# Optimization experiments

Measured on AMD Instinct MI355X. Metric: run time of the kernel, lower is better.

Reference implementation:

```python
import jax, jax.numpy as jnp
import numpy as np

B, T, E, H, R = 1, 2048, 4096, 16, 64
D = E // H
SCALE_ATTN = float(np.sqrt(D))


def _i8_linear(x, W, b, alpha, beta):
    # W8A8B8O8Linear: int8 in, int8 weight/bias, int8 out with requant epilogue
    acc = jnp.einsum('bte,oe->bto', x.astype(jnp.int32), W.astype(jnp.int32)).astype(jnp.float32)
    y = alpha * acc + beta * b.astype(jnp.float32)
    return jnp.clip(jnp.round(y), -128, 127).astype(jnp.int8)


def _rotate_every_two(x):
    x1, x2 = x[..., ::2], x[..., 1::2]
    return jnp.stack([-x2, x1], axis=-1).reshape(x.shape)


def _sincos(seq_len, dim):
    inv_freq = 1.0 / (10000.0 ** (jnp.arange(0, dim, 2, dtype=jnp.float32) / dim))
    ang = jnp.arange(seq_len, dtype=jnp.float32)[:, None] * inv_freq[None, :]
    return jnp.sin(ang), jnp.cos(ang)


def _apply_rotary(x, sin, cos):
    # duplicate_interleave -> repeat each freq twice along last dim
    sin = jnp.repeat(sin, 2, axis=-1)[None, :, None, :]
    cos = jnp.repeat(cos, 2, axis=-1)[None, :, None, :]
    return x * cos + _rotate_every_two(x) * sin


def setup_inputs():
    key = jax.random.key(0)
    ks = jax.random.split(key, 9)
    i8 = lambda k, s: jax.random.randint(k, s, -128, 128, dtype=jnp.int32).astype(jnp.int8)
    return {
        'hidden_states': i8(ks[0], (B, T, E)),
        'Wq': i8(ks[1], (E, E)), 'bq': i8(ks[2], (E,)),
        'Wk': i8(ks[3], (E, E)), 'bk': i8(ks[4], (E,)),
        'Wv': i8(ks[5], (E, E)), 'bv': i8(ks[6], (E,)),
        'Wo': i8(ks[7], (E, E)),
        'b_out': jax.random.normal(ks[8], (E,), dtype=jnp.float32),
        'alpha_q': 2e-4, 'beta_q': 1.0,
        'alpha_k': 2e-4, 'beta_k': 1.0,
        'alpha_v': 2e-4, 'beta_v': 1.0,
        'alpha_qk': 1e-3, 'alpha_pv': 1e-2, 'alpha_out': 2e-4,
    }


def reference(hidden_states, Wq, bq, Wk, bk, Wv, bv, Wo, b_out,
              alpha_q, beta_q, alpha_k, beta_k, alpha_v, beta_v,
              alpha_qk, alpha_pv, alpha_out):
    # int8 q/k/v projections -> [B, T, H, D]
    q = _i8_linear(hidden_states, Wq, bq, alpha_q, beta_q).reshape(B, T, H, D)
    k = _i8_linear(hidden_states, Wk, bk, alpha_k, beta_k).reshape(B, T, H, D)
    v = _i8_linear(hidden_states, Wv, bv, alpha_v, beta_v).reshape(B, T, H, D)
    v = v.transpose(0, 2, 1, 3)  # [B, H, T, D] int8

    # fused rotary on first R dims (float math on dequantized-per-tensor int8 codes)
    sin, cos = _sincos(T, R)
    qf, kf = q.astype(jnp.float32), k.astype(jnp.float32)
    qf = jnp.concatenate([_apply_rotary(qf[..., :R], sin, cos), qf[..., R:]], axis=-1)
    kf = jnp.concatenate([_apply_rotary(kf[..., :R], sin, cos), kf[..., R:]], axis=-1)
    # torch .to(int8) truncates toward zero
    to_i8 = lambda x: jnp.clip(jnp.trunc(x), -128, 127).astype(jnp.int8)
    q = to_i8(qf.transpose(0, 2, 1, 3))  # [B, H, T, D]
    k = to_i8(kf.transpose(0, 2, 1, 3))

    scores = alpha_qk * jnp.einsum('bhtd,bhsd->bhts', q.astype(jnp.int32), k.astype(jnp.int32)).astype(jnp.float32)
    causal = jnp.tril(jnp.ones((T, T), dtype=bool))
    scores = jnp.where(causal, scores, jnp.finfo(jnp.float32).min)
    probs = jax.nn.softmax(scores / SCALE_ATTN, axis=-1)
    probs = jnp.round(probs * 127.0).astype(jnp.int8)  # requant probs to int8

    acc = jnp.einsum('bhts,bhsd->bhtd', probs.astype(jnp.int32), v.astype(jnp.int32)).astype(jnp.float32)
    attn_out = jnp.clip(jnp.round(alpha_pv * acc), -128, 127).astype(jnp.int8)
    attn_out = attn_out.transpose(0, 2, 1, 3).reshape(B, T, E)  # merge heads

    # W8A8BFP32OFP32Linear
    out = alpha_out * jnp.einsum('bte,oe->bto', attn_out.astype(jnp.int32), Wo.astype(jnp.int32)).astype(jnp.float32) + b_out
    return out
```

## Files before the change

kernel.cpp:

```cpp
#include <hip/hip_runtime.h>
#include <cstdint>
#include <cmath>

#define T_ 2048
#define E_ 4096
#define H_ 16
#define D_ 256
#define NF 32

typedef int v4i  __attribute__((ext_vector_type(4)));

__device__ __forceinline__ int dot4(int a, int b, int c) {
#if __has_builtin(__builtin_amdgcn_sdot4)
  return __builtin_amdgcn_sdot4(a, b, c, false);
#else
  c += ((a << 24) >> 24) * ((b << 24) >> 24);
  c += ((a << 16) >> 24) * ((b << 16) >> 24);
  c += ((a <<  8) >> 24) * ((b <<  8) >> 24);
  c += (a >> 24) * (b >> 24);
  return c;
#endif
}

__device__ __forceinline__ int pack4i(int4 v) {
  return (v.x & 255) | ((v.y & 255) << 8) | ((v.z & 255) << 16) | (v.w << 24);
}

#define GLD_LDS16(g, l)                                                        \
  __builtin_amdgcn_global_load_lds(                                            \
      (const __attribute__((address_space(1))) void*)(g),                      \
      (__attribute__((address_space(3))) void*)(l), 16, 0, 0)

__global__ void sincos_kernel(float* __restrict__ sinT, float* __restrict__ cosT) {
  int idx = blockIdx.x * 256 + threadIdx.x;
  int t = idx >> 5, j = idx & 31;
  float invf = (float)exp(-(double)j * (log(10000.0) / 32.0));
  float ang = (float)t * invf;
  sinT[idx] = (float)sin((double)ang);
  cosT[idx] = (float)cos((double)ang);
}

__global__ __launch_bounds__(256) void repack_kernel(const int* __restrict__ src,
                                                     int8_t* __restrict__ dst) {
  size_t i = (size_t)blockIdx.x * 256 + threadIdx.x;
  const int4* s = (const int4*)src + i * 4;
  int4 a = s[0], b = s[1], c = s[2], d = s[3];
  int4 o;
  o.x = pack4i(a); o.y = pack4i(b); o.z = pack4i(c); o.w = pack4i(d);
  ((int4*)dst)[i] = o;
}

__global__ __launch_bounds__(256) void qkv_gemm_mfma(
    const int8_t* __restrict__ x8,
    const int8_t* __restrict__ Wq8, const int* __restrict__ bq,
    const int8_t* __restrict__ Wk8, const int* __restrict__ bk,
    const int8_t* __restrict__ Wv8, const int* __restrict__ bv,
    const float* __restrict__ alpq, const float* __restrict__ betq,
    const float* __restrict__ alpk, const float* __restrict__ betk,
    const float* __restrict__ alpv, const float* __restrict__ betv,
    int8_t* __restrict__ Q8, int8_t* __restrict__ K8, int8_t* __restrict__ VT)
{
  const int mode = blockIdx.z;
  const int8_t* __restrict__ W = (mode == 0) ? Wq8 : (mode == 1 ? Wk8 : Wv8);
  const int* __restrict__ bs   = (mode == 0) ? bq  : (mode == 1 ? bk  : bv);
  const float alpha = (mode == 0) ? alpq[0] : (mode == 1 ? alpk[0] : alpv[0]);
  const float beta  = (mode == 0) ? betq[0] : (mode == 1 ? betk[0] : betv[0]);

  __shared__ int8_t As[128 * 64];
  __shared__ int8_t Bs[128 * 64];

  const int tid  = threadIdx.x;
  const int wave = tid >> 6, lane = tid & 63;
  const int wm = wave >> 1, wn = wave & 1;
  const int t0 = blockIdx.x * 128, o0 = blockIdx.y * 128;

  const int srow = lane >> 2;
  const int scol = (lane & 3) * 16;
  const int col  = lane & 15;
  const int quad = lane >> 4;

  v4i acc[4][4] = {};

  const int8_t* gA0 = x8 + (size_t)(t0 + wave * 32 + srow) * E_ + scol;
  const int8_t* gB0 = W  + (size_t)(o0 + wave * 32 + srow) * E_ + scol;

  for (int e0 = 0; e0 < E_; e0 += 64) {
    __syncthreads();
    GLD_LDS16(gA0 + e0,                 As + wave * 2048);
    GLD_LDS16(gA0 + e0 + 16 * E_,       As + wave * 2048 + 1024);
    GLD_LDS16(gB0 + e0,                 Bs + wave * 2048);
    GLD_LDS16(gB0 + e0 + 16 * E_,       Bs + wave * 2048 + 1024);
    __syncthreads();

    v4i a[4], b[4];
    #pragma unroll
    for (int i = 0; i < 4; ++i)
      a[i] = *(const v4i*)(As + (wm * 64 + i * 16 + col) * 64 + quad * 16);
    #pragma unroll
    for (int j = 0; j < 4; ++j)
      b[j] = *(const v4i*)(Bs + (wn * 64 + j * 16 + col) * 64 + quad * 16);
    #pragma unroll
    for (int i = 0; i < 4; ++i)
      #pragma unroll
      for (int j = 0; j < 4; ++j)
        acc[i][j] = __builtin_amdgcn_mfma_i32_16x16x64_i8(a[i], b[j], acc[i][j], 0, 0, 0);
  }

  int8_t* __restrict__ dst = (mode == 0) ? Q8 : (mode == 1 ? K8 : VT);
  #pragma unroll
  for (int j = 0; j < 4; ++j) {
    const int o  = o0 + wn * 64 + j * 16 + col;
    const int h  = o >> 8;
    const int dd = o & 255;
    const float bb = (float)bs[o];
    #pragma unroll
    for (int i = 0; i < 4; ++i) {
      const int tb = t0 + wm * 64 + i * 16 + quad * 4;
      int qb[4];
      #pragma unroll
      for (int r = 0; r < 4; ++r) {
        float v = __fadd_rn(__fmul_rn(alpha, (float)acc[i][j][r]),
                            __fmul_rn(beta, bb));
        v = rintf(v);
        v = fminf(fmaxf(v, -128.0f), 127.0f);
        qb[r] = (int)v;
      }
      if (mode == 2) {
        int packed = (qb[0] & 255) | ((qb[1] & 255) << 8) |
                     ((qb[2] & 255) << 16) | ((qb[3] & 255) << 24);
        *(int*)(dst + ((size_t)h * 256 + dd) * T_ + tb) = packed;
      } else {
        #pragma unroll
        for (int r = 0; r < 4; ++r)
          dst[((size_t)h * T_ + tb + r) * D_ + dd] = (int8_t)qb[r];
      }
    }
  }
}

__global__ __launch_bounds__(256) void rope_kernel(
    int8_t* __restrict__ Q8, int8_t* __restrict__ K8,
    const float* __restrict__ sinT, const float* __restrict__ cosT)
{
  int idx = blockIdx.x * 256 + threadIdx.x;
  int c = idx & 3;
  int t = (idx >> 2) & (T_ - 1);
  int h = (idx >> 13) & (H_ - 1);
  int m = idx >> 17;
  int8_t* base = (m == 0 ? Q8 : K8) + ((size_t)h * T_ + t) * D_ + c * 16;
  int4 v = *(int4*)base;
  int u[4] = {v.x, v.y, v.z, v.w};
  const int jb = c * 8;
  #pragma unroll
  for (int ui = 0; ui < 4; ++ui) {
    const int j = jb + ui * 2;
    const float s0 = sinT[t * NF + j],     c0 = cosT[t * NF + j];
    const float s1 = sinT[t * NF + j + 1], c1 = cosT[t * NF + j + 1];
    const int w = u[ui];
    float y0 = (float)((w << 24) >> 24);
    float y1 = (float)((w << 16) >> 24);
    float y2 = (float)((w <<  8) >> 24);
    float y3 = (float)(w >> 24);
    float r0 = __fadd_rn(__fmul_rn(y0, c0), __fmul_rn(-y1, s0));
    float r1 = __fadd_rn(__fmul_rn(y1, c0), __fmul_rn( y0, s0));
    float r2 = __fadd_rn(__fmul_rn(y2, c1), __fmul_rn(-y3, s1));
    float r3 = __fadd_rn(__fmul_rn(y3, c1), __fmul_rn( y2, s1));
    int q0 = (int)fminf(fmaxf(truncf(r0), -128.0f), 127.0f);
    int q1 = (int)fminf(fmaxf(truncf(r1), -128.0f), 127.0f);
    int q2 = (int)fminf(fmaxf(truncf(r2), -128.0f), 127.0f);
    int q3 = (int)fminf(fmaxf(truncf(r3), -128.0f), 127.0f);
    u[ui] = (q0 & 255) | ((q1 & 255) << 8) | ((q2 & 255) << 16) | ((q3 & 255) << 24);
  }
  int4 ov; ov.x = u[0]; ov.y = u[1]; ov.z = u[2]; ov.w = u[3];
  *(int4*)base = ov;
}

__global__ __launch_bounds__(256) void out_gemm_mfma(
    const int8_t* __restrict__ xa, const int8_t* __restrict__ Wo8,
    const float* __restrict__ b_out, const float* __restrict__ p_aout,
    float* __restrict__ out)
{
  const float alpha = p_aout[0];
  __shared__ int8_t As[128 * 64];
  __shared__ int8_t Bs[128 * 64];

  const int tid  = threadIdx.x;
  const int wave = tid >> 6, lane = tid & 63;
  const int wm = wave >> 1, wn = wave & 1;
  const int t0 = blockIdx.x * 128, o0 = blockIdx.y * 128;
  const int srow = lane >> 2, scol = (lane & 3) * 16;
  const int col = lane & 15, quad = lane >> 4;

  v4i acc[4][4] = {};
  const int8_t* gA0 = xa  + (size_t)(t0 + wave * 32 + srow) * E_ + scol;
  const int8_t* gB0 = Wo8 + (size_t)(o0 + wave * 32 + srow) * E_ + scol;

  for (int e0 = 0; e0 < E_; e0 += 64) {
    __syncthreads();
    GLD_LDS16(gA0 + e0,            As + wave * 2048);
    GLD_LDS16(gA0 + e0 + 16 * E_,  As + wave * 2048 + 1024);
    GLD_LDS16(gB0 + e0,            Bs + wave * 2048);
    GLD_LDS16(gB0 + e0 + 16 * E_,  Bs + wave * 2048 + 1024);
    __syncthreads();

    v4i a[4], b[4];
    #pragma unroll
    for (int i = 0; i < 4; ++i)
      a[i] = *(const v4i*)(As + (wm * 64 + i * 16 + col) * 64 + quad * 16);
    #pragma unroll
    for (int j = 0; j < 4; ++j)
      b[j] = *(const v4i*)(Bs + (wn * 64 + j * 16 + col) * 64 + quad * 16);
    #pragma unroll
    for (int i = 0; i < 4; ++i)
      #pragma unroll
      for (int j = 0; j < 4; ++j)
        acc[i][j] = __builtin_amdgcn_mfma_i32_16x16x64_i8(a[i], b[j], acc[i][j], 0, 0, 0);
  }

  #pragma unroll
  for (int j = 0; j < 4; ++j) {
    const int o = o0 + wn * 64 + j * 16 + col;
    const float bb = b_out[o];
    #pragma unroll
    for (int i = 0; i < 4; ++i) {
      #pragma unroll
      for (int r = 0; r < 4; ++r) {
        const int t = t0 + wm * 64 + i * 16 + quad * 4 + r;
        out[(size_t)t * E_ + o] = __fadd_rn(__fmul_rn(alpha, (float)acc[i][j][r]), bb);
      }
    }
  }
}

__global__ __launch_bounds__(256) void attn_mfma(
    const int8_t* __restrict__ Q8, const int8_t* __restrict__ K8,
    const int8_t* __restrict__ VT,
    const float* __restrict__ p_aqk, const float* __restrict__ p_apv,
    int8_t* __restrict__ attn8)
{
  __shared__ int8_t Qs[4 * 4096];
  __shared__ int8_t KVs[16384];
  __shared__ int8_t Ps[64][64];
  __shared__ float  mred[64][2];
  __shared__ float  sred[64][2];

  const int h   = blockIdx.y;
  const int t0  = blockIdx.x * 64;
  const int tid = threadIdx.x;
  const int wave = tid >> 6, lane = tid & 63;
  const int wm = wave >> 1, wn = wave & 1;
  const int col = lane & 15, quad = lane >> 4;
  const int srow = lane >> 2, scol = (lane & 3) * 16;
  const float aqk = p_aqk[0] * 0.0625f;
  const float apv = p_apv[0];

  {
    const int8_t* g = Q8 + ((size_t)h * T_ + t0 + wave * 16 + srow) * D_ + scol;
    #pragma unroll
    for (int c = 0; c < 4; ++c)
      GLD_LDS16(g + c * 64, Qs + c * 4096 + wave * 1024);
  }

  const int nt = t0 / 64 + 1;

  float m[8], sm[8];
  #pragma unroll
  for (int u = 0; u < 8; ++u) { m[u] = -INFINITY; sm[u] = 0.0f; }

  for (int it = 0; it < nt; ++it) {
    const int s0 = it * 64;
    __syncthreads();
    {
      const int8_t* g = K8 + ((size_t)h * T_ + s0 + wave * 16 + srow) * D_ + scol;
      #pragma unroll
      for (int c = 0; c < 4; ++c)
        GLD_LDS16(g + c * 64, KVs + c * 4096 + wave * 1024);
    }
    __syncthreads();
    v4i accS[2][2] = {};
    #pragma unroll
    for (int c = 0; c < 4; ++c) {
      v4i a[2], b[2];
      #pragma unroll
      for (int i = 0; i < 2; ++i)
        a[i] = *(const v4i*)(Qs + c * 4096 + (wm * 32 + i * 16 + col) * 64 + quad * 16);
      #pragma unroll
      for (int j = 0; j < 2; ++j)
        b[j] = *(const v4i*)(KVs + c * 4096 + (wn * 32 + j * 16 + col) * 64 + quad * 16);
      #pragma unroll
      for (int i = 0; i < 2; ++i)
        #pragma unroll
        for (int j = 0; j < 2; ++j)
          accS[i][j] = __builtin_amdgcn_mfma_i32_16x16x64_i8(a[i], b[j], accS[i][j], 0, 0, 0);
    }
    const bool diag = (s0 == t0);
    #pragma unroll
    for (int i = 0; i < 2; ++i) {
      #pragma unroll
      for (int r = 0; r < 4; ++r) {
        const int ri = i * 4 + r;
        const int qrow = t0 + wm * 32 + i * 16 + quad * 4 + r;
        #pragma unroll
        for (int j = 0; j < 2; ++j) {
          const int s = s0 + wn * 32 + j * 16 + col;
          if (!diag || s <= qrow) {
            float l = __fmul_rn(aqk, (float)accS[i][j][r]);
            if (l > m[ri]) { sm[ri] = sm[ri] * expf(m[ri] - l) + 1.0f; m[ri] = l; }
            else           { sm[ri] += expf(l - m[ri]); }
          }
        }
      }
    }
  }

  #pragma unroll
  for (int u = 0; u < 8; ++u) {
    #pragma unroll
    for (int off = 1; off < 16; off <<= 1) {
      float om = __shfl_xor(m[u], off);
      float os = __shfl_xor(sm[u], off);
      float mm = fmaxf(m[u], om);
      float e1 = (m[u] == mm) ? 1.0f : expf(m[u] - mm);
      float e2 = (om   == mm) ? 1.0f : expf(om - mm);
      sm[u] = sm[u] * e1 + os * e2;
      m[u] = mm;
    }
  }
  __syncthreads();
  if (col == 0) {
    #pragma unroll
    for (int u = 0; u < 8; ++u) {
      int row = wm * 32 + (u >> 2) * 16 + quad * 4 + (u & 3);
      mred[row][wn] = m[u];
      sred[row][wn] = sm[u];
    }
  }
  __syncthreads();
  float mF[8], sF[8];
  #pragma unroll
  for (int u = 0; u < 8; ++u) {
    int row = wm * 32 + (u >> 2) * 16 + quad * 4 + (u & 3);
    float m0 = mred[row][0], m1 = mred[row][1];
    float sa = sred[row][0], sb = sred[row][1];
    float mm = fmaxf(m0, m1);
    float e0 = (m0 == mm) ? 1.0f : expf(m0 - mm);
    float e1 = (m1 == mm) ? 1.0f : expf(m1 - mm);
    mF[u] = mm;
    sF[u] = __fadd_rn(__fmul_rn(sa, e0), __fmul_rn(sb, e1));
  }

  v4i pv[2][8] = {};
  for (int it = 0; it < nt; ++it) {
    const int s0 = it * 64;
    __syncthreads();
    {
      const int8_t* g = K8 + ((size_t)h * T_ + s0 + wave * 16 + srow) * D_ + scol;
      #pragma unroll
      for (int c = 0; c < 4; ++c)
        GLD_LDS16(g + c * 64, KVs + c * 4096 + wave * 1024);
    }
    __syncthreads();
    v4i accS[2][2] = {};
    #pragma unroll
    for (int c = 0; c < 4; ++c) {
      v4i a[2], b[2];
      #pragma unroll
      for (int i = 0; i < 2; ++i)
        a[i] = *(const v4i*)(Qs + c * 4096 + (wm * 32 + i * 16 + col) * 64 + quad * 16);
      #pragma unroll
      for (int j = 0; j < 2; ++j)
        b[j] = *(const v4i*)(KVs + c * 4096 + (wn * 32 + j * 16 + col) * 64 + quad * 16);
      #pragma unroll
      for (int i = 0; i < 2; ++i)
        #pragma unroll
        for (int j = 0; j < 2; ++j)
          accS[i][j] = __builtin_amdgcn_mfma_i32_16x16x64_i8(a[i], b[j], accS[i][j], 0, 0, 0);
    }
    __syncthreads();
    {
      #pragma unroll
      for (int c = 0; c < 4; ++c) {
        const int drow = (wave * 4 + c) * 16 + srow;
        GLD_LDS16(VT + ((size_t)h * 256 + drow) * T_ + s0 + scol,
                  KVs + (wave * 4 + c) * 1024);
      }
    }
    const bool diag = (s0 == t0);
    #pragma unroll
    for (int i = 0; i < 2; ++i) {
      #pragma unroll
      for (int r = 0; r < 4; ++r) {
        const int ri = i * 4 + r;
        const int qrow = t0 + wm * 32 + i * 16 + quad * 4 + r;
        #pragma unroll
        for (int j = 0; j < 2; ++j) {
          const int s = s0 + wn * 32 + j * 16 + col;
          int q = 0;
          if (!diag || s <= qrow) {
            float l = __fmul_rn(aqk, (float)accS[i][j][r]);
            float p = expf(l - mF[ri]) / sF[ri];
            q = (int)rintf(__fmul_rn(p, 127.0f));
          }
          Ps[wm * 32 + i * 16 + quad * 4 + r][wn * 32 + j * 16 + col] = (int8_t)q;
        }
      }
    }
    __syncthreads();
    v4i a2[2], b2[8];
    #pragma unroll
    for (int i = 0; i < 2; ++i)
      a2[i] = *(const v4i*)&Ps[wm * 32 + i * 16 + col][quad * 16];
    #pragma unroll
    for (int dt = 0; dt < 8; ++dt)
      b2[dt] = *(const v4i*)(KVs + (wn * 128 + dt * 16 + col) * 64 + quad * 16);
    #pragma unroll
    for (int i = 0; i < 2; ++i)
      #pragma unroll
      for (int dt = 0; dt < 8; ++dt)
        pv[i][dt] = __builtin_amdgcn_mfma_i32_16x16x64_i8(a2[i], b2[dt], pv[i][dt], 0, 0, 0);
  }

  #pragma unroll
  for (int i = 0; i < 2; ++i) {
    #pragma unroll
    for (int r = 0; r < 4; ++r) {
      const int t = t0 + wm * 32 + i * 16 + quad * 4 + r;
      #pragma unroll
      for (int dt = 0; dt < 8; ++dt) {
        const int d = wn * 128 + dt * 16 + col;
        float y = rintf(__fmul_rn(apv, (float)pv[i][dt][r]));
        y = fminf(fmaxf(y, -128.0f), 127.0f);
        attn8[(size_t)t * E_ + h * D_ + d] = (int8_t)(int)y;
      }
    }
  }
}

__global__ __launch_bounds__(256) void qkv_gemm_fb(
    const int* __restrict__ xp,
    const int* __restrict__ Wqp, const int* __restrict__ bq,
    const int* __restrict__ Wkp, const int* __restrict__ bk,
    const int* __restrict__ Wvp, const int* __restrict__ bv,
    const float* __restrict__ alpq, const float* __restrict__ betq,
    const float* __restrict__ alpk, const float* __restrict__ betk,
    const float* __restrict__ alpv, const float* __restrict__ betv,
    const float* __restrict__ sinT, const float* __restrict__ cosT,
    int8_t* __restrict__ Q8, int8_t* __restrict__ K8, int8_t* __restrict__ VT)
{
  const int mode = blockIdx.z;
  const int* __restrict__ Wp = (mode == 0) ? Wqp : (mode == 1 ? Wkp : Wvp);
  const int* __restrict__ bs = (mode == 0) ? bq  : (mode == 1 ? bk  : bv);
  const float alpha = (mode == 0) ? alpq[0] : (mode == 1 ? alpk[0] : alpv[0]);
  const float beta  = (mode == 0) ? betq[0] : (mode == 1 ? betk[0] : betv[0]);

  __shared__ int As[64 * 17];
  __shared__ int Bs[64 * 17];
  const int tid = threadIdx.x;
  const int tx = tid & 15, ty = tid >> 4;
  const int t0 = blockIdx.x * 64, o0 = blockIdx.y * 64;
  const int lrow = tid >> 2, lc = tid & 3;
  int acc[4][4] = {};

  for (int e0 = 0; e0 < E_; e0 += 64) {
    const int* xr = xp + (size_t)(t0 + lrow) * E_ + e0 + lc * 16;
    const int* wr = Wp + (size_t)(o0 + lrow) * E_ + e0 + lc * 16;
    int a4[4], b4[4];
    #pragma unroll
    for (int u = 0; u < 4; ++u) a4[u] = pack4i(((const int4*)xr)[u]);
    #pragma unroll
    for (int u = 0; u < 4; ++u) b4[u] = pack4i(((const int4*)wr)[u]);
    __syncthreads();
    int* ap = &As[lrow * 17 + lc * 4];
    ap[0] = a4[0]; ap[1] = a4[1]; ap[2] = a4[2]; ap[3] = a4[3];
    int* bp = &Bs[lrow * 17 + lc * 4];
    bp[0] = b4[0]; bp[1] = b4[1]; bp[2] = b4[2]; bp[3] = b4[3];
    __syncthreads();
    #pragma unroll
    for (int kk = 0; kk < 16; ++kk) {
      int a[4], b[4];
      #pragma unroll
      for (int i = 0; i < 4; ++i) a[i] = As[(ty * 4 + i) * 17 + kk];
      #pragma unroll
      for (int j = 0; j < 4; ++j) b[j] = Bs[(tx * 4 + j) * 17 + kk];
      #pragma unroll
      for (int i = 0; i < 4; ++i)
        #pragma unroll
        for (int j = 0; j < 4; ++j)
          acc[i][j] = dot4(a[i], b[j], acc[i][j]);
    }
  }

  const int ob = o0 + tx * 4;
  const int h  = ob >> 8;
  const int dd = ob & 255;
  #pragma unroll
  for (int i = 0; i < 4; ++i) {
    const int t = t0 + ty * 4 + i;
    float y[4];
    #pragma unroll
    for (int j = 0; j < 4; ++j) {
      float v = __fadd_rn(__fmul_rn(alpha, (float)acc[i][j]),
                          __fmul_rn(beta, (float)bs[ob + j]));
      v = rintf(v);
      y[j] = fminf(fmaxf(v, -128.0f), 127.0f);
    }
    int q0, q1, q2, q3;
    if (mode < 2 && dd < 64) {
      const int j0 = dd >> 1;
      const float s0 = sinT[t * NF + j0],     c0 = cosT[t * NF + j0];
      const float s1 = sinT[t * NF + j0 + 1], c1 = cosT[t * NF + j0 + 1];
      float r0 = __fadd_rn(__fmul_rn(y[0], c0), __fmul_rn(-y[1], s0));
      float r1 = __fadd_rn(__fmul_rn(y[1], c0), __fmul_rn( y[0], s0));
      float r2 = __fadd_rn(__fmul_rn(y[2], c1), __fmul_rn(-y[3], s1));
      float r3 = __fadd_rn(__fmul_rn(y[3], c1), __fmul_rn( y[2], s1));
      q0 = (int)fminf(fmaxf(truncf(r0), -128.0f), 127.0f);
      q1 = (int)fminf(fmaxf(truncf(r1), -128.0f), 127.0f);
      q2 = (int)fminf(fmaxf(truncf(r2), -128.0f), 127.0f);
      q3 = (int)fminf(fmaxf(truncf(r3), -128.0f), 127.0f);
    } else {
      q0 = (int)y[0]; q1 = (int)y[1]; q2 = (int)y[2]; q3 = (int)y[3];
    }
    if (mode == 2) {
      VT[((size_t)h * 256 + dd + 0) * T_ + t] = (int8_t)q0;
      VT[((size_t)h * 256 + dd + 1) * T_ + t] = (int8_t)q1;
      VT[((size_t)h * 256 + dd + 2) * T_ + t] = (int8_t)q2;
      VT[((size_t)h * 256 + dd + 3) * T_ + t] = (int8_t)q3;
    } else {
      int8_t* dst = (mode == 0) ? Q8 : K8;
      int packed = (q0 & 255) | ((q1 & 255) << 8) | ((q2 & 255) << 16) | ((q3 & 255) << 24);
      *(int*)(dst + ((size_t)h * T_ + t) * D_ + dd) = packed;
    }
  }
}

__global__ __launch_bounds__(256) void out_gemm_fb(
    const int8_t* __restrict__ xa, const int* __restrict__ Wop,
    const float* __restrict__ b_out, const float* __restrict__ p_aout,
    float* __restrict__ out)
{
  __shared__ int As[64 * 17];
  __shared__ int Bs[64 * 17];
  const float alpha = p_aout[0];
  const int tid = threadIdx.x;
  const int tx = tid & 15, ty = tid >> 4;
  const int t0 = blockIdx.x * 64, o0 = blockIdx.y * 64;
  const int lrow = tid >> 2, lc = tid & 3;
  int acc[4][4] = {};

  for (int e0 = 0; e0 < E_; e0 += 64) {
    int4 av4 = *(const int4*)(xa + (size_t)(t0 + lrow) * E_ + e0 + lc * 16);
    const int* wr = Wop + (size_t)(o0 + lrow) * E_ + e0 + lc * 16;
    int b4[4];
    #pragma unroll
    for (int u = 0; u < 4; ++u) b4[u] = pack4i(((const int4*)wr)[u]);
    __syncthreads();
    int* ap = &As[lrow * 17 + lc * 4];
    ap[0] = av4.x; ap[1] = av4.y; ap[2] = av4.z; ap[3] = av4.w;
    int* bp = &Bs[lrow * 17 + lc * 4];
    bp[0] = b4[0]; bp[1] = b4[1]; bp[2] = b4[2]; bp[3] = b4[3];
    __syncthreads();
    #pragma unroll
    for (int kk = 0; kk < 16; ++kk) {
      int a[4], b[4];
      #pragma unroll
      for (int i = 0; i < 4; ++i) a[i] = As[(ty * 4 + i) * 17 + kk];
      #pragma unroll
      for (int j = 0; j < 4; ++j) b[j] = Bs[(tx * 4 + j) * 17 + kk];
      #pragma unroll
      for (int i = 0; i < 4; ++i)
        #pragma unroll
        for (int j = 0; j < 4; ++j)
          acc[i][j] = dot4(a[i], b[j], acc[i][j]);
    }
  }
  #pragma unroll
  for (int i = 0; i < 4; ++i) {
    const int t = t0 + ty * 4 + i;
    const int ob = o0 + tx * 4;
    #pragma unroll
    for (int j = 0; j < 4; ++j) {
      out[(size_t)t * E_ + ob + j] =
          __fadd_rn(__fmul_rn(alpha, (float)acc[i][j]), b_out[ob + j]);
    }
  }
}

extern "C" void kernel_launch(void* const* d_in, const int* in_sizes, int n_in,
                              void* d_out, int out_size, void* d_ws, size_t ws_size,
                              hipStream_t stream) {
  const int* hs   = (const int*)d_in[0];
  const int* Wq   = (const int*)d_in[1];
  const int* bq   = (const int*)d_in[2];
  const int* Wk   = (const int*)d_in[3];
  const int* bk   = (const int*)d_in[4];
  const int* Wv   = (const int*)d_in[5];
  const int* bv   = (const int*)d_in[6];
  const int* Wo   = (const int*)d_in[7];
  const float* b_out = (const float*)d_in[8];
  const float* aq   = (const float*)d_in[9];
  const float* btq  = (const float*)d_in[10];
  const float* ak   = (const float*)d_in[11];
  const float* btk  = (const float*)d_in[12];
  const float* av   = (const float*)d_in[13];
  const float* btv  = (const float*)d_in[14];
  const float* aqk  = (const float*)d_in[15];
  const float* apv  = (const float*)d_in[16];
  const float* aout = (const float*)d_in[17];

  const size_t SEG = (size_t)H_ * T_ * D_;
  char* ws = (char*)d_ws;
  int8_t* Q8    = (int8_t*)ws;
  int8_t* K8    = Q8 + SEG;
  int8_t* VT    = K8 + SEG;
  int8_t* attn8 = VT + SEG;
  int8_t* x8    = attn8;
  float*  sinT  = (float*)(ws + 4 * SEG);
  float*  cosT  = sinT + T_ * NF;
  int8_t* Wq8   = (int8_t*)(cosT + T_ * NF);
  int8_t* Wk8   = Wq8 + (size_t)E_ * E_;
  int8_t* Wv8   = Wk8 + (size_t)E_ * E_;
  int8_t* Wo8   = Wv8 + (size_t)E_ * E_;
  const size_t NEED = 4 * SEG + 2 * (size_t)T_ * NF * 4 + 4 * (size_t)E_ * E_;
  const bool big = (ws_size >= NEED);

  sincos_kernel<<<(T_ * NF) / 256, 256, 0, stream>>>(sinT, cosT);

  if (big) {
    repack_kernel<<<(T_ * E_ / 16) / 256, 256, 0, stream>>>(hs, x8);
    repack_kernel<<<(E_ * E_ / 16) / 256, 256, 0, stream>>>(Wq, Wq8);
    repack_kernel<<<(E_ * E_ / 16) / 256, 256, 0, stream>>>(Wk, Wk8);
    repack_kernel<<<(E_ * E_ / 16) / 256, 256, 0, stream>>>(Wv, Wv8);
    repack_kernel<<<(E_ * E_ / 16) / 256, 256, 0, stream>>>(Wo, Wo8);
    qkv_gemm_mfma<<<dim3(T_ / 128, E_ / 128, 3), 256, 0, stream>>>(
        x8, Wq8, bq, Wk8, bk, Wv8, bv, aq, btq, ak, btk, av, btv, Q8, K8, VT);
    rope_kernel<<<(2 * H_ * T_ * 4) / 256, 256, 0, stream>>>(Q8, K8, sinT, cosT);
  } else {
    qkv_gemm_fb<<<dim3(T_ / 64, E_ / 64, 3), 256, 0, stream>>>(
        hs, Wq, bq, Wk, bk, Wv, bv, aq, btq, ak, btk, av, btv,
        sinT, cosT, Q8, K8, VT);
  }

  attn_mfma<<<dim3(T_ / 64, H_), 256, 0, stream>>>(Q8, K8, VT, aqk, apv, attn8);

  if (big) {
    out_gemm_mfma<<<dim3(T_ / 128, E_ / 128), 256, 0, stream>>>(
        attn8, Wo8, b_out, aout, (float*)d_out);
  } else {
    out_gemm_fb<<<dim3(T_ / 64, E_ / 64), 256, 0, stream>>>(
        attn8, Wo, b_out, aout, (float*)d_out);
  }
}
```

Measured before the change: 687.3 us.

## Split causal attention into chunked max/sum and PV passes with combine kernels

Replaces the single attention kernel (one block per 64-query tile per head) with a split-K style pipeline. A chunked kernel computes partial row max and sum over groups of 4 key tiles, a combine kernel merges them, a second chunked kernel recomputes scores and accumulates int32 P·V over up to 16 key tiles, and a final kernel sums the partials and requantizes. The goal is more parallelism and better load balance across the causal triangle, since the old kernel's 512 blocks had very uneven work. In exchange QK^T is computed twice, there are extra launches and global partial traffic, and dead weight buffers are reused as scratch space.

```diff
diff --git a/kernel.cpp b/kernel.cpp
--- a/kernel.cpp
+++ b/kernel.cpp
@@ -230,6 +230,311 @@
       }
     }
   }
+}
+
+__global__ __launch_bounds__(256) void attn_ms_chunk(
+    const int8_t* __restrict__ Q8, const int8_t* __restrict__ K8,
+    const float* __restrict__ p_aqk,
+    float* __restrict__ mPart, float* __restrict__ sPart)
+{
+  const int ch = blockIdx.x;
+  const int qi = blockIdx.y;
+  const int h  = blockIdx.z;
+  if ((ch << 2) > qi) return;
+
+  __shared__ int8_t Qs[4 * 4096];
+  __shared__ int8_t KVs[16384];
+  __shared__ float  mred[64][2];
+  __shared__ float  sred[64][2];
+
+  const int t0  = qi * 64;
+  const int tid = threadIdx.x;
+  const int wave = tid >> 6, lane = tid & 63;
+  const int wm = wave >> 1, wn = wave & 1;
+  const int col = lane & 15, quad = lane >> 4;
+  const int srow = lane >> 2, scol = (lane & 3) * 16;
+  const float aqk = p_aqk[0] * 0.0625f;
+
+  {
+    const int8_t* g = Q8 + ((size_t)h * T_ + t0 + wave * 16 + srow) * D_ + scol;
+    #pragma unroll
+    for (int c = 0; c < 4; ++c)
+      GLD_LDS16(g + c * 64, Qs + c * 4096 + wave * 1024);
+  }
+
+  const int it0 = ch * 4;
+  const int it1 = (it0 + 3 < qi) ? (it0 + 3) : qi;
+
+  float m[8], sm[8];
+  #pragma unroll
+  for (int u = 0; u < 8; ++u) { m[u] = -INFINITY; sm[u] = 0.0f; }
+
+  for (int it = it0; it <= it1; ++it) {
+    const int s0 = it * 64;
+    __syncthreads();
+    {
+      const int8_t* g = K8 + ((size_t)h * T_ + s0 + wave * 16 + srow) * D_ + scol;
+      #pragma unroll
+      for (int c = 0; c < 4; ++c)
+        GLD_LDS16(g + c * 64, KVs + c * 4096 + wave * 1024);
+    }
+    __syncthreads();
+    v4i accS[2][2] = {};
+    #pragma unroll
+    for (int c = 0; c < 4; ++c) {
+      v4i a[2], b[2];
+      #pragma unroll
+      for (int i = 0; i < 2; ++i)
+        a[i] = *(const v4i*)(Qs + c * 4096 + (wm * 32 + i * 16 + col) * 64 + quad * 16);
+      #pragma unroll
+      for (int j = 0; j < 2; ++j)
+        b[j] = *(const v4i*)(KVs + c * 4096 + (wn * 32 + j * 16 + col) * 64 + quad * 16);
+      #pragma unroll
+      for (int i = 0; i < 2; ++i)
+        #pragma unroll
+        for (int j = 0; j < 2; ++j)
+          accS[i][j] = __builtin_amdgcn_mfma_i32_16x16x64_i8(a[i], b[j], accS[i][j], 0, 0, 0);
+    }
+    const bool diag = (s0 == t0);
+    #pragma unroll
+    for (int i = 0; i < 2; ++i) {
+      #pragma unroll
+      for (int r = 0; r < 4; ++r) {
+        const int ri = i * 4 + r;
+        const int qrow = t0 + wm * 32 + i * 16 + quad * 4 + r;
+        #pragma unroll
+        for (int j = 0; j < 2; ++j) {
+          const int s = s0 + wn * 32 + j * 16 + col;
+          if (!diag || s <= qrow) {
+            float l = __fmul_rn(aqk, (float)accS[i][j][r]);
+            if (l > m[ri]) { sm[ri] = sm[ri] * expf(m[ri] - l) + 1.0f; m[ri] = l; }
+            else           { sm[ri] += expf(l - m[ri]); }
+          }
+        }
+      }
+    }
+  }
+
+  #pragma unroll
+  for (int u = 0; u < 8; ++u) {
+    #pragma unroll
+    for (int off = 1; off < 16; off <<= 1) {
+      float om = __shfl_xor(m[u], off);
+      float os = __shfl_xor(sm[u], off);
+      float mm = fmaxf(m[u], om);
+      float e1 = (m[u] == mm) ? 1.0f : expf(m[u] - mm);
+      float e2 = (om   == mm) ? 1.0f : expf(om - mm);
+      sm[u] = sm[u] * e1 + os * e2;
+      m[u] = mm;
+    }
+  }
+  __syncthreads();
+  if (col == 0) {
+    #pragma unroll
+    for (int u = 0; u < 8; ++u) {
+      int row = wm * 32 + (u >> 2) * 16 + quad * 4 + (u & 3);
+      mred[row][wn] = m[u];
+      sred[row][wn] = sm[u];
+    }
+  }
+  __syncthreads();
+  if (col == 0 && wn == 0) {
+    #pragma unroll
+    for (int u = 0; u < 8; ++u) {
+      int row = wm * 32 + (u >> 2) * 16 + quad * 4 + (u & 3);
+      float m0 = mred[row][0], m1 = mred[row][1];
+      float sa = sred[row][0], sb = sred[row][1];
+      float mm = fmaxf(m0, m1);
+      float e0 = (m0 == mm) ? 1.0f : expf(m0 - mm);
+      float e1 = (m1 == mm) ? 1.0f : expf(m1 - mm);
+      size_t base = (((size_t)h * 32 + qi) * 64 + row) * 8 + ch;
+      mPart[base] = mm;
+      sPart[base] = __fadd_rn(__fmul_rn(sa, e0), __fmul_rn(sb, e1));
+    }
+  }
+}
+
+__global__ __launch_bounds__(256) void attn_ms_combine(
+    const float* __restrict__ mPart, const float* __restrict__ sPart,
+    float* __restrict__ mFg, float* __restrict__ sFg)
+{
+  int idx = blockIdx.x * 256 + threadIdx.x;
+  int t = idx & (T_ - 1), h = idx >> 11;
+  int qi = t >> 6, row = t & 63;
+  int nch = (qi >> 2) + 1;
+  const float* mp = mPart + (((size_t)h * 32 + qi) * 64 + row) * 8;
+  const float* sp = sPart + (((size_t)h * 32 + qi) * 64 + row) * 8;
+  float m = mp[0], s = sp[0];
+  for (int c = 1; c < nch; ++c) {
+    float mc = mp[c], sc = sp[c];
+    float mm = fmaxf(m, mc);
+    float e1 = (m  == mm) ? 1.0f : expf(m - mm);
+    float e2 = (mc == mm) ? 1.0f : expf(mc - mm);
+    s = __fadd_rn(__fmul_rn(s, e1), __fmul_rn(sc, e2));
+    m = mm;
+  }
+  mFg[idx] = m;
+  sFg[idx] = s;
+}
+
+__global__ __launch_bounds__(256) void attn_pv_chunk(
+    const int8_t* __restrict__ Q8, const int8_t* __restrict__ K8,
+    const int8_t* __restrict__ VT,
+    const float* __restrict__ p_aqk,
+    const float* __restrict__ mFg, const float* __restrict__ sFg,
+    int* __restrict__ P0, int* __restrict__ P1)
+{
+  const int cc = blockIdx.x;
+  const int qi = 31 - blockIdx.y;
+  const int h  = blockIdx.z;
+  if (cc == 1 && qi < 16) return;
+
+  __shared__ int8_t Qs[4 * 4096];
+  __shared__ int8_t KVs[16384];
+  __shared__ int8_t Ps[64][64];
+
+  const int t0  = qi * 64;
+  const int tid = threadIdx.x;
+  const int wave = tid >> 6, lane = tid & 63;
+  const int wm = wave >> 1, wn = wave & 1;
+  const int col = lane & 15, quad = lane >> 4;
+  const int srow = lane >> 2, scol = (lane & 3) * 16;
+  const float aqk = p_aqk[0] * 0.0625f;
+
+  {
+    const int8_t* g = Q8 + ((size_t)h * T_ + t0 + wave * 16 + srow) * D_ + scol;
+    #pragma unroll
+    for (int c = 0; c < 4; ++c)
+      GLD_LDS16(g + c * 64, Qs + c * 4096 + wave * 1024);
+  }
+
+  float mF[8], sF[8];
+  #pragma unroll
+  for (int u = 0; u < 8; ++u) {
+    const int row = wm * 32 + (u >> 2) * 16 + quad * 4 + (u & 3);
+    mF[u] = mFg[h * T_ + t0 + row];
+    sF[u] = sFg[h * T_ + t0 + row];
+  }
+
+  const int it0 = cc * 16;
+  const int it1 = (it0 + 15 < qi) ? (it0 + 15) : qi;
+
+  v4i pv[2][8] = {};
+  for (int it = it0; it <= it1; ++it) {
+    const int s0 = it * 64;
+    __syncthreads();
+    {
+      const int8_t* g = K8 + ((size_t)h * T_ + s0 + wave * 16 + srow) * D_ + scol;
+      #pragma unroll
+      for (int c = 0; c < 4; ++c)
+        GLD_LDS16(g + c * 64, KVs + c * 4096 + wave * 1024);
+    }
+    __syncthreads();
+    v4i accS[2][2] = {};
+    #pragma unroll
+    for (int c = 0; c < 4; ++c) {
+      v4i a[2], b[2];
+      #pragma unroll
+      for (int i = 0; i < 2; ++i)
+        a[i] = *(const v4i*)(Qs + c * 4096 + (wm * 32 + i * 16 + col) * 64 + quad * 16);
+      #pragma unroll
+      for (int j = 0; j < 2; ++j)
+        b[j] = *(const v4i*)(KVs + c * 4096 + (wn * 32 + j * 16 + col) * 64 + quad * 16);
+      #pragma unroll
+      for (int i = 0; i < 2; ++i)
+        #pragma unroll
+        for (int j = 0; j < 2; ++j)
+          accS[i][j] = __builtin_amdgcn_mfma_i32_16x16x64_i8(a[i], b[j], accS[i][j], 0, 0, 0);
+    }
+    __syncthreads();
+    {
+      #pragma unroll
+      for (int c = 0; c < 4; ++c) {
+        const int drow = (wave * 4 + c) * 16 + srow;
+        GLD_LDS16(VT + ((size_t)h * 256 + drow) * T_ + s0 + scol,
+                  KVs + (wave * 4 + c) * 1024);
+      }
+    }
+    const bool diag = (s0 == t0);
+    #pragma unroll
+    for (int i = 0; i < 2; ++i) {
+      #pragma unroll
+      for (int r = 0; r < 4; ++r) {
+        const int ri = i * 4 + r;
+        const int qrow = t0 + wm * 32 + i * 16 + quad * 4 + r;
+        #pragma unroll
+        for (int j = 0; j < 2; ++j) {
+          const int s = s0 + wn * 32 + j * 16 + col;
+          int q = 0;
+          if (!diag || s <= qrow) {
+            float l = __fmul_rn(aqk, (float)accS[i][j][r]);
+            float p = expf(l - mF[ri]) / sF[ri];
+            q = (int)rintf(__fmul_rn(p, 127.0f));
+          }
+          Ps[wm * 32 + i * 16 + quad * 4 + r][wn * 32 + j * 16 + col] = (int8_t)q;
+        }
+      }
+    }
+    __syncthreads();
+    v4i a2[2], b2[8];
+    #pragma unroll
+    for (int i = 0; i < 2; ++i)
+      a2[i] = *(const v4i*)&Ps[wm * 32 + i * 16 + col][quad * 16];
+    #pragma unroll
+    for (int dt = 0; dt < 8; ++dt)
+      b2[dt] = *(const v4i*)(KVs + (wn * 128 + dt * 16 + col) * 64 + quad * 16);
+    #pragma unroll
+    for (int i = 0; i < 2; ++i)
+      #pragma unroll
+      for (int dt = 0; dt < 8; ++dt)
+        pv[i][dt] = __builtin_amdgcn_mfma_i32_16x16x64_i8(a2[i], b2[dt], pv[i][dt], 0, 0, 0);
+  }
+
+  int* __restrict__ dst = (cc == 0)
+      ? P0 + (((size_t)h * 32 + qi) << 14)
+      : P1 + (((size_t)h * 16 + (qi - 16)) << 14);
+  #pragma unroll
+  for (int i = 0; i < 2; ++i) {
+    #pragma unroll
+    for (int r = 0; r < 4; ++r) {
+      const int trow = wm * 32 + i * 16 + quad * 4 + r;
+      #pragma unroll
+      for (int dt = 0; dt < 8; ++dt) {
+        const int d = wn * 128 + dt * 16 + col;
+        dst[trow * 256 + d] = pv[i][dt][r];
+      }
+    }
+  }
+}
+
+__global__ __launch_bounds__(256) void attn_pv_combine(
+    const int* __restrict__ P0, const int* __restrict__ P1,
+    const float* __restrict__ p_apv, int8_t* __restrict__ attn8)
+{
+  const float apv = p_apv[0];
+  int idx = blockIdx.x * 256 + threadIdx.x;
+  int d4  = idx & 63;
+  int row = (idx >> 6) & 63;
+  int qi  = (idx >> 12) & 31;
+  int h   = idx >> 17;
+  size_t off = (((size_t)h * 32 + qi) << 14) + row * 256 + d4 * 4;
+  int4 a = *(const int4*)(P0 + off);
+  if (qi >= 16) {
+    size_t off1 = (((size_t)h * 16 + (qi - 16)) << 14) + row * 256 + d4 * 4;
+    int4 b1 = *(const int4*)(P1 + off1);
+    a.x += b1.x; a.y += b1.y; a.z += b1.z; a.w += b1.w;
+  }
+  int q[4];
+  int vv[4] = {a.x, a.y, a.z, a.w};
+  #pragma unroll
+  for (int r = 0; r < 4; ++r) {
+    float y = rintf(__fmul_rn(apv, (float)vv[r]));
+    y = fminf(fmaxf(y, -128.0f), 127.0f);
+    q[r] = (int)y;
+  }
+  int packed = (q[0] & 255) | ((q[1] & 255) << 8) | ((q[2] & 255) << 16) | ((q[3] & 255) << 24);
+  int t = qi * 64 + row;
+  *(int*)(attn8 + (size_t)t * E_ + h * D_ + d4 * 4) = packed;
 }
 
 __global__ __launch_bounds__(256) void attn_mfma(
@@ -634,18 +939,28 @@
     qkv_gemm_mfma<<<dim3(T_ / 128, E_ / 128, 3), 256, 0, stream>>>(
         x8, Wq8, bq, Wk8, bk, Wv8, bv, aq, btq, ak, btk, av, btv, Q8, K8, VT);
     rope_kernel<<<(2 * H_ * T_ * 4) / 256, 256, 0, stream>>>(Q8, K8, sinT, cosT);
+
+    int*   P1g   = (int*)Wq8;
+    int*   P0g   = (int*)Wk8;
+    float* mPart = (float*)attn8;
+    float* sPart = mPart + (size_t)H_ * 32 * 64 * 8;
+    float* mFg   = sPart + (size_t)H_ * 32 * 64 * 8;
+    float* sFg   = mFg + (size_t)H_ * T_;
+
+    attn_ms_chunk<<<dim3(8, 32, H_), 256, 0, stream>>>(Q8, K8, aqk, mPart, sPart);
+    attn_ms_combine<<<(H_ * T_) / 256, 256, 0, stream>>>(mPart, sPart, mFg, sFg);
+    attn_pv_chunk<<<dim3(2, 32, H_), 256, 0, stream>>>(
+        Q8, K8, VT, aqk, mFg, sFg, P0g, P1g);
+    attn_pv_combine<<<(H_ * 32 * 64 * 64) / 256, 256, 0, stream>>>(
+        P0g, P1g, apv, attn8);
+
+    out_gemm_mfma<<<dim3(T_ / 128, E_ / 128), 256, 0, stream>>>(
+        attn8, Wo8, b_out, aout, (float*)d_out);
   } else {
     qkv_gemm_fb<<<dim3(T_ / 64, E_ / 64, 3), 256, 0, stream>>>(
         hs, Wq, bq, Wk, bk, Wv, bv, aq, btq, ak, btk, av, btv,
         sinT, cosT, Q8, K8, VT);
-  }
-
-  attn_mfma<<<dim3(T_ / 64, H_), 256, 0, stream>>>(Q8, K8, VT, aqk, apv, attn8);
-
-  if (big) {
-    out_gemm_mfma<<<dim3(T_ / 128, E_ / 128), 256, 0, stream>>>(
-        attn8, Wo8, b_out, aout, (float*)d_out);
-  } else {
+    attn_mfma<<<dim3(T_ / 64, H_), 256, 0, stream>>>(Q8, K8, VT, aqk, apv, attn8);
     out_gemm_fb<<<dim3(T_ / 64, E_ / 64), 256, 0, stream>>>(
         attn8, Wo, b_out, aout, (float*)d_out);
   }
```

After: 701.3 us. 1.02x slower.
